# Optimization experiments

Hardware: AMD Instinct MI355X
Metric: run time of the kernel (lower is better)

The kernel has to match this reference:

```python
import jax, jax.numpy as jnp
import numpy as np

N_NODES = 100000
N_EDGES = 3200000
G_EDGES = 1600000
D_FEAT = 256
K_CLUSTERS = 16
COLLAPSE_REG = 0.1


def setup_inputs() -> dict:
    key = jax.random.key(0)
    ks = jax.random.split(key, 12)
    inp = {
        'features': jax.random.normal(ks[0], (N_NODES, D_FEAT), dtype=jnp.float32),
        'W': jax.random.normal(ks[1], (D_FEAT, K_CLUSTERS), dtype=jnp.float32) / np.sqrt(D_FEAT),
        'b': jnp.zeros((K_CLUSTERS,), dtype=jnp.float32),
        'adj_src': jax.random.randint(ks[2], (N_EDGES,), 0, N_NODES, dtype=jnp.int32),
        'adj_dst': jax.random.randint(ks[3], (N_EDGES,), 0, N_NODES, dtype=jnp.int32),
        'adj_val': jax.random.uniform(ks[4], (N_EDGES,), dtype=jnp.float32),
        'g1_src': jax.random.randint(ks[5], (G_EDGES,), 0, N_NODES, dtype=jnp.int32),
        'g1_dst': jax.random.randint(ks[6], (G_EDGES,), 0, N_NODES, dtype=jnp.int32),
        'g1_val': jax.random.uniform(ks[7], (G_EDGES,), dtype=jnp.float32),
        'g2_src': jax.random.randint(ks[8], (G_EDGES,), 0, N_NODES, dtype=jnp.int32),
        'g2_dst': jax.random.randint(ks[9], (G_EDGES,), 0, N_NODES, dtype=jnp.int32),
        'g2_val': jax.random.uniform(ks[10], (G_EDGES,), dtype=jnp.float32),
        'lamda': 1,
    }
    return inp


def _spmm(src, dst, val, X, n):
    # (sparse A) @ X where A[src, dst] = val : out[i] = sum_j A[i,j] X[j]
    return jax.ops.segment_sum(val[:, None] * X[dst], src, num_segments=n)


def _col_degrees(src, dst, val, n):
    # tf.sparse.reduce_sum(A, axis=0): column sums
    return jax.ops.segment_sum(val, dst, num_segments=n)


def reference(features, W, b, adj_src, adj_dst, adj_val,
              g1_src, g1_dst, g1_val, g2_src, g2_dst, g2_val, lamda):
    n = features.shape[0]
    k = W.shape[1]
    # soft cluster assignments  [n, k]
    S = jax.nn.softmax(features @ W + b, axis=1)
    cluster_sizes = jnp.sum(S, axis=0)            # [k]
    S_pool = S / cluster_sizes                    # [n, k]

    # full-graph modularity
    deg = _col_degrees(adj_src, adj_dst, adj_val, n)  # [n]
    m = jnp.sum(deg)                                  # total edge weight
    AS = _spmm(adj_src, adj_dst, adj_val, S, n)       # [n, k]
    graph_pooled = AS.T @ S                           # [k, k]
    dS = deg @ S                                      # [k] = S^T deg
    normalizer = jnp.outer(dS, dS) / 2.0 / m          # [k, k]
    spectral_loss = -jnp.trace(graph_pooled - normalizer) / 2.0 / m

    # per-group modularity Q_g
    def group_Q(src, dst, val):
        gdeg = _col_degrees(src, dst, val, n)
        gm = jnp.sum(gdeg)
        safe_gm = jnp.where(gm > 0, gm, 1.0)
        gAS = _spmm(src, dst, val, S, n)
        g_pooled = gAS.T @ S
        gdS = gdeg @ S
        g_norm = jnp.outer(gdS, gdS) / 2.0 / safe_gm
        Qg = jnp.trace(g_pooled - g_norm) / 2.0 / m
        return jnp.where(gm > 0, Qg, 0.0), gm

    Q1, m1 = group_Q(g1_src, g1_dst, g1_val)
    Q2, m2 = group_Q(g2_src, g2_dst, g2_val)
    Q_min = jnp.minimum(Q1, Q2)
    g_edges_mean = (m1 + m2) / 2.0
    edge_ratio = m / (g_edges_mean + 1e-8)
    fairness_loss = edge_ratio * (-Q_min)

    collapse_loss = (jnp.linalg.norm(cluster_sizes) / n) * jnp.sqrt(jnp.float32(k)) - 1.0

    total_loss = spectral_loss + lamda * fairness_loss + COLLAPSE_REG * collapse_loss

    features_pooled = jax.nn.selu(S_pool.T @ features)  # [k, d]
    return features_pooled, S, total_loss
```

## Files before the change

### kernel.cpp

```cpp
#include <hip/hip_runtime.h>
#include <cstddef>
#include <cstdint>


#define G1_MAX   1024
#define EGRID    2048
#define NSEG     16
#define OFF_E    0
#define SZ_E     (3 * 18 * EGRID)
#define OFF_R    (OFF_E + SZ_E)
#define OFF_G    (OFF_R + 4112)
#define OFF_F8   (OFF_G + 64)

#define TROWS    32
#define RPAD2    134

#define BLK0     384
#define BLK12    192

typedef int      iv4 __attribute__((ext_vector_type(4)));
typedef float    fv4 __attribute__((ext_vector_type(4)));
typedef _Float16 hh;
typedef hh       h2  __attribute__((ext_vector_type(2)));

#if __has_builtin(__builtin_amdgcn_cvt_pk_f32_fp8)
#define HW_FP8 1
#endif

__device__ __forceinline__ h2 bch2(unsigned u) { return __builtin_bit_cast(h2, u); }

__device__ __forceinline__ float fdot2(h2 a, h2 b, float c)
{
#if __has_builtin(__builtin_amdgcn_fdot2)
    return __builtin_amdgcn_fdot2(a, b, c, false);
#else
    return fmaf((float)a[0], (float)b[0], fmaf((float)a[1], (float)b[1], c));
#endif
}

__device__ __forceinline__ h2 pk16(float x, float y)
{
#if __has_builtin(__builtin_amdgcn_cvt_pkrtz)
    return __builtin_bit_cast(h2, __builtin_amdgcn_cvt_pkrtz(x, y));
#else
    h2 r; r[0] = (hh)x; r[1] = (hh)y; return r;
#endif
}

__device__ __forceinline__ unsigned f32_to_e4m3(float f)
{
    unsigned bits = __float_as_uint(f);
    unsigned s = bits >> 31;
    int e32 = (int)((bits >> 23) & 255);
    unsigned m23 = bits & 0x7FFFFF;
    int e = e32 - 120;
    unsigned out;
    if (e32 == 0) out = 0;
    else if (e <= 0) {
        float av = fabsf(f);
        int q = (int)(av * 512.0f + 0.5f);
        out = (unsigned)q;
    } else if (e > 15) out = (15u << 3) | 6u;
    else {
        unsigned m3 = (m23 + 0x80000u) >> 20;
        if (m3 == 8u) { m3 = 0u; ++e; if (e > 15) { e = 15; m3 = 6u; } }
        out = ((unsigned)e << 3) | m3;
    }
    return out | (s << 7);
}

__device__ __forceinline__ void decode16(uint4 r, float* o, const float* lut)
{
#ifdef HW_FP8
    #pragma unroll
    for (int j = 0; j < 4; ++j) {
        unsigned u = (&r.x)[j];
        auto lo = __builtin_amdgcn_cvt_pk_f32_fp8(u, false);
        auto hi = __builtin_amdgcn_cvt_pk_f32_fp8(u, true);
        o[4*j]   = lo[0]; o[4*j+1] = lo[1];
        o[4*j+2] = hi[0]; o[4*j+3] = hi[1];
    }
#else
    #pragma unroll
    for (int j = 0; j < 4; ++j) {
        unsigned u = (&r.x)[j];
        #pragma unroll
        for (int q = 0; q < 4; ++q)
            o[4*j+q] = lut[(u >> (8*q)) & 255];
    }
#endif
}

__global__ void __launch_bounds__(256)
k_rows(const float* __restrict__ F, const float* __restrict__ W,
       const float* __restrict__ b, float* __restrict__ S_out,
       unsigned* __restrict__ S_f8, float* __restrict__ ws_P, int n, int n_tiles)
{
    __shared__ h2    Wt_h2[16][RPAD2];
    __shared__ h2    rows_h2[TROWS][RPAD2];
    __shared__ float S_lds[TROWS][17];
    __shared__ float cs_red[256];

    const int t = threadIdx.x;

    for (int idx = t; idx < 2048; idx += 256) {
        int k = idx & 15, p = idx >> 4;
        Wt_h2[k][p] = pk16(W[(2*p) * 16 + k], W[(2*p + 1) * 16 + k]);
    }

    const float bk = b[t & 15];
    const int rl = t >> 4;
    const int kl = t & 15;
    const int kp = t & 15;
    const int cp = t >> 4;

    h2 Pa[8];
    #pragma unroll
    for (int j = 0; j < 8; ++j) Pa[j] = pk16(0.f, 0.f);
    float cs_acc = 0.f;
    __syncthreads();

    for (int tile = blockIdx.x; tile < n_tiles; tile += gridDim.x) {
        const int row0 = tile * TROWS;
        const float4* F4 = (const float4*)(F + (size_t)row0 * 256);
        #pragma unroll
        for (int q = 0; q < 8; ++q) {
            int idx = t + (q << 8);
            int r = idx >> 6, c4 = idx & 63;
            float4 v = {0.f, 0.f, 0.f, 0.f};
            if (row0 + r < n) v = F4[idx];
            rows_h2[r][c4 * 2]     = pk16(v.x, v.y);
            rows_h2[r][c4 * 2 + 1] = pk16(v.z, v.w);
        }
        __syncthreads();

        float a0 = 0.f, a1 = 0.f;
        #pragma unroll 8
        for (int dd = 0; dd < 32; ++dd) {
            uint4 wv = *(const uint4*)&Wt_h2[kl][dd << 2];
            uint4 r0 = *(const uint4*)&rows_h2[rl][dd << 2];
            uint4 r1 = *(const uint4*)&rows_h2[rl + 16][dd << 2];
            #pragma unroll
            for (int j = 0; j < 4; ++j) {
                h2 wj = bch2((&wv.x)[j]);
                a0 = fdot2(wj, bch2((&r0.x)[j]), a0);
                a1 = fdot2(wj, bch2((&r1.x)[j]), a1);
            }
        }
        a0 += bk; a1 += bk;

        float mx0 = a0, mx1 = a1;
        #pragma unroll
        for (int o = 8; o; o >>= 1) {
            mx0 = fmaxf(mx0, __shfl_xor(mx0, o, 16));
            mx1 = fmaxf(mx1, __shfl_xor(mx1, o, 16));
        }
        float e0 = __expf(a0 - mx0), e1 = __expf(a1 - mx1);
        float s0 = e0, s1 = e1;
        #pragma unroll
        for (int o = 8; o; o >>= 1) {
            s0 += __shfl_xor(s0, o, 16);
            s1 += __shfl_xor(s1, o, 16);
        }
        float sv0 = e0 / s0, sv1 = e1 / s1;

        const bool v0 = (row0 + rl) < n;
        const bool v1 = (row0 + rl + 16) < n;
        if (v0) { S_out[(((size_t)(row0 + rl)) << 4) + kl] = sv0; cs_acc += sv0; }
        if (v1) { S_out[(((size_t)(row0 + rl + 16)) << 4) + kl] = sv1; cs_acc += sv1; }
        S_lds[rl][kl]      = v0 ? sv0 : 0.f;
        S_lds[rl + 16][kl] = v1 ? sv1 : 0.f;
        __syncthreads();

        if (t < 128) {
            int r = t >> 2, c = t & 3;
            int row = row0 + r;
            if (row < n) {
                unsigned u = f32_to_e4m3(S_lds[r][4*c])
                           | (f32_to_e4m3(S_lds[r][4*c+1]) << 8)
                           | (f32_to_e4m3(S_lds[r][4*c+2]) << 16)
                           | (f32_to_e4m3(S_lds[r][4*c+3]) << 24);
                S_f8[((size_t)row << 2) + c] = u;
            }
        }

        #pragma unroll 4
        for (int r = 0; r < TROWS; ++r) {
            float sv = S_lds[r][kp];
            h2 svh = pk16(sv, sv);
            uint4 fa = *(const uint4*)&rows_h2[r][cp << 3];
            uint4 fb = *(const uint4*)&rows_h2[r][(cp << 3) + 4];
            #pragma unroll
            for (int j = 0; j < 4; ++j) {
                Pa[j]     = svh * bch2((&fa.x)[j]) + Pa[j];
                Pa[4 + j] = svh * bch2((&fb.x)[j]) + Pa[4 + j];
            }
        }
        __syncthreads();
    }

    {
        float o16[16];
        #pragma unroll
        for (int j = 0; j < 8; ++j) {
            o16[2*j]     = (float)Pa[j][0];
            o16[2*j + 1] = (float)Pa[j][1];
        }
        float* dst = ws_P + (size_t)blockIdx.x * 4112 + kp * 256 + (cp << 4);
        #pragma unroll
        for (int j = 0; j < 4; ++j)
            *(float4*)&dst[4*j] = make_float4(o16[4*j], o16[4*j+1], o16[4*j+2], o16[4*j+3]);
    }
    cs_red[t] = cs_acc;
    __syncthreads();
    if (t < 16) {
        float ssum = 0.f;
        #pragma unroll
        for (int i = 0; i < 16; ++i) ssum += cs_red[t + (i << 4)];
        ws_P[(size_t)blockIdx.x * 4112 + 4096 + t] = ssum;
    }
}

__global__ void __launch_bounds__(256)
k_reduce(const float* __restrict__ ws_P, float* __restrict__ ws_red, int nb)
{
    const int seg  = blockIdx.x & (NSEG - 1);
    const int jblk = blockIdx.x / NSEG;
    const int idx  = jblk * 256 + threadIdx.x;
    if (idx >= 4112) return;
    const int chunk = (nb + NSEG - 1) / NSEG;
    const int b0 = seg * chunk;
    const int b1 = min(nb, b0 + chunk);
    float s = 0.f;
    for (int bb = b0; bb < b1; ++bb)
        s += ws_P[(size_t)bb * 4112 + idx];
    atomicAdd(&ws_red[idx], s);
}

__global__ void __launch_bounds__(256, 2)
k_edge(const int* __restrict__ src0, const int* __restrict__ dst0,
       const float* __restrict__ val0, int n0,
       const int* __restrict__ src1, const int* __restrict__ dst1,
       const float* __restrict__ val1, int n1,
       const int* __restrict__ src2, const int* __restrict__ dst2,
       const float* __restrict__ val2, int n2,
       const uint4* __restrict__ S8, float* __restrict__ ws_e,
       int b0, int b1)
{
#ifndef HW_FP8
    __shared__ float lut[256];
    if (threadIdx.x < 256) {
        int i = threadIdx.x;
        int e_ = (i >> 3) & 15, m_ = i & 7, s_ = i >> 7;
        float v = e_ ? ldexpf((float)(8 + m_), e_ - 10) : ldexpf((float)m_, -9);
        lut[i] = s_ ? -v : v;
    }
    __syncthreads();
    const float* lutp = lut;
#else
    const float* lutp = nullptr;
#endif

    int g, bb, nblk, nE;
    const int* src; const int* dst; const float* val;
    if ((int)blockIdx.x < b0)      { g = 0; bb = blockIdx.x;      nblk = b0;             src = src0; dst = dst0; val = val0; nE = n0; }
    else if ((int)blockIdx.x < b1) { g = 1; bb = blockIdx.x - b0; nblk = b1 - b0;        src = src1; dst = dst1; val = val1; nE = n1; }
    else                           { g = 2; bb = blockIdx.x - b1; nblk = gridDim.x - b1; src = src2; dst = dst2; val = val2; nE = n2; }

    float m_acc = 0.f, tr_acc = 0.f;
    float gds[16];
    #pragma unroll
    for (int k = 0; k < 16; ++k) gds[k] = 0.f;

    const int nv = nE >> 3;
    const iv4* s4 = (const iv4*)src;
    const iv4* d4 = (const iv4*)dst;
    const fv4* v4 = (const fv4*)val;
    const int stride = nblk * 256;

    for (int i = bb * 256 + threadIdx.x; i < nv; i += stride) {
        iv4 sa = __builtin_nontemporal_load(&s4[2*i]);
        iv4 sb = __builtin_nontemporal_load(&s4[2*i+1]);
        iv4 da = __builtin_nontemporal_load(&d4[2*i]);
        iv4 db = __builtin_nontemporal_load(&d4[2*i+1]);
        fv4 va = __builtin_nontemporal_load(&v4[2*i]);
        fv4 vb = __builtin_nontemporal_load(&v4[2*i+1]);
        int   is[8] = {sa[0], sa[1], sa[2], sa[3], sb[0], sb[1], sb[2], sb[3]};
        int   id[8] = {da[0], da[1], da[2], da[3], db[0], db[1], db[2], db[3]};
        float vv[8] = {va[0], va[1], va[2], va[3], vb[0], vb[1], vb[2], vb[3]};
        uint4 rs[8], rd[8];
        #pragma unroll
        for (int e = 0; e < 8; ++e) {
            rs[e] = S8[is[e]];
            rd[e] = S8[id[e]];
        }
        #pragma unroll
        for (int e = 0; e < 8; ++e) {
            float sv[16], dv[16];
            decode16(rs[e], sv, lutp);
            decode16(rd[e], dv, lutp);
            float v = vv[e];
            float dot = 0.f;
            #pragma unroll
            for (int k = 0; k < 16; ++k) dot = fmaf(sv[k], dv[k], dot);
            m_acc += v;
            tr_acc = fmaf(v, dot, tr_acc);
            #pragma unroll
            for (int k = 0; k < 16; ++k) gds[k] = fmaf(v, dv[k], gds[k]);
        }
    }

    if (bb == 0) {
        int e = (nv << 3) + threadIdx.x;
        if (e < nE) {
            float sv[16], dv[16];
            decode16(S8[src[e]], sv, lutp);
            decode16(S8[dst[e]], dv, lutp);
            float v = val[e];
            float dot = 0.f;
            #pragma unroll
            for (int k = 0; k < 16; ++k) dot = fmaf(sv[k], dv[k], dot);
            m_acc += v;
            tr_acc = fmaf(v, dot, tr_acc);
            #pragma unroll
            for (int k = 0; k < 16; ++k) gds[k] = fmaf(v, dv[k], gds[k]);
        }
    }

    #pragma unroll
    for (int o = 32; o; o >>= 1) {
        m_acc  += __shfl_xor(m_acc, o);
        tr_acc += __shfl_xor(tr_acc, o);
        #pragma unroll
        for (int k = 0; k < 16; ++k) gds[k] += __shfl_xor(gds[k], o);
    }
    __shared__ float wred[4][18];
    const int wid = threadIdx.x >> 6, lane = threadIdx.x & 63;
    if (lane == 0) {
        wred[wid][0] = m_acc; wred[wid][1] = tr_acc;
        #pragma unroll
        for (int k = 0; k < 16; ++k) wred[wid][2 + k] = gds[k];
    }
    __syncthreads();
    if (threadIdx.x < 18) {
        float s = wred[0][threadIdx.x] + wred[1][threadIdx.x]
                + wred[2][threadIdx.x] + wred[3][threadIdx.x];
        ws_e[(size_t)g * 18 * EGRID + (size_t)threadIdx.x * EGRID + bb] = s;
    }
}

__global__ void __launch_bounds__(256)
k_ereduce(const float* __restrict__ ws_e, float* __restrict__ G54,
          int g0, int g1, int g2)
{
    const int p = blockIdx.x;
    const int g = p / 18, slot = p % 18;
    int grids[3] = {g0, g1, g2};
    const int gb = grids[g];
    const float* base = ws_e + (size_t)g * 18 * EGRID + (size_t)slot * EGRID;

    const int t = threadIdx.x;
    float s = 0.f;
    for (int bb = t; bb < gb; bb += 256) s += base[bb];
    #pragma unroll
    for (int o = 32; o; o >>= 1) s += __shfl_xor(s, o);

    __shared__ float wr[4];
    if ((t & 63) == 0) wr[t >> 6] = s;
    __syncthreads();
    if (t == 0) G54[p] = wr[0] + wr[1] + wr[2] + wr[3];
}

__global__ void __launch_bounds__(256)
k_final(const float* __restrict__ ws_red, const float* __restrict__ G54,
        const void* __restrict__ lamda_ptr, float* __restrict__ out, int n)
{
    __shared__ float G[54];
    const int t = threadIdx.x;
    if (t < 54) G[t] = G54[t];
    __syncthreads();

    const float* P  = ws_red;
    const float* cs = ws_red + 4096;

    const float scale = 1.0507009873554805f;
    const float alpha = 1.6732632423543772f;
    for (int idx = t; idx < 4096; idx += 256) {
        int k = idx >> 8;
        float x = P[idx] / cs[k];
        float y = x > 0.f ? scale * x : scale * alpha * (expf(x) - 1.f);
        out[idx] = y;
    }

    if (t == 0) {
        int   li = *(const int*)lamda_ptr;
        float lf = *(const float*)lamda_ptr;
        float lamda = (li > -100000 && li < 100000) ? (float)li : lf;

        float m = G[0], trA = G[1];
        float ds2 = 0.f;
        for (int k = 0; k < 16; ++k) ds2 += G[2 + k] * G[2 + k];
        float spectral = -(trA - ds2 / (2.f * m)) / (2.f * m);

        float Q[2], gm[2];
        for (int g = 0; g < 2; ++g) {
            const float* Gg = G + 18 * (g + 1);
            float mg = Gg[0], trg = Gg[1];
            float gds2 = 0.f;
            for (int k = 0; k < 16; ++k) gds2 += Gg[2 + k] * Gg[2 + k];
            float safe = mg > 0.f ? mg : 1.f;
            float q = (trg - gds2 / (2.f * safe)) / (2.f * m);
            Q[g]  = mg > 0.f ? q : 0.f;
            gm[g] = mg;
        }
        float Qmin = fminf(Q[0], Q[1]);
        float gmean = 0.5f * (gm[0] + gm[1]);
        float fairness = (m / (gmean + 1e-8f)) * (-Qmin);

        float csn = 0.f;
        for (int k = 0; k < 16; ++k) csn += cs[k] * cs[k];
        float collapse = (sqrtf(csn) / (float)n) * 4.f - 1.f;

        out[4096 + (size_t)n * 16] = spectral + lamda * fairness + 0.1f * collapse;
    }
}

extern "C" void kernel_launch(void* const* d_in, const int* in_sizes, int n_in,
                              void* d_out, int out_size, void* d_ws, size_t ws_size,
                              hipStream_t stream)
{
    const float* F       = (const float*)d_in[0];
    const float* W       = (const float*)d_in[1];
    const float* b       = (const float*)d_in[2];
    const int*   adj_src = (const int*)d_in[3];
    const int*   adj_dst = (const int*)d_in[4];
    const float* adj_val = (const float*)d_in[5];
    const int*   g1_src  = (const int*)d_in[6];
    const int*   g1_dst  = (const int*)d_in[7];
    const float* g1_val  = (const float*)d_in[8];
    const int*   g2_src  = (const int*)d_in[9];
    const int*   g2_dst  = (const int*)d_in[10];
    const float* g2_val  = (const float*)d_in[11];
    const void*  lamda_p = d_in[12];

    const int n  = in_sizes[0] / 256;
    const int nE = in_sizes[3];
    const int n1 = in_sizes[6];
    const int n2 = in_sizes[9];

    float* out   = (float*)d_out;
    float* S_out = out + 4096;

    float* ws   = (float*)d_ws;
    float* ws_e = ws + OFF_E;
    float* ws_r = ws + OFF_R;
    float* ws_g = ws + OFF_G;
    unsigned* S8 = (unsigned*)(ws + OFF_F8);
    const size_t off_p = (size_t)OFF_F8 + (size_t)n * 4;
    float* ws_P = ws + off_p;

    const int n_tiles = (n + TROWS - 1) / TROWS;
    long avail = ((long)(ws_size / 4) - (long)off_p) / 4112;
    int grid1 = n_tiles < G1_MAX ? n_tiles : G1_MAX;
    if (avail < grid1) grid1 = (int)avail;
    if (grid1 < 1) grid1 = 1;

    (void)hipMemsetAsync(ws_r, 0, 4112 * sizeof(float), stream);

    k_rows<<<grid1, 256, 0, stream>>>(F, W, b, S_out, S8, ws_P, n, n_tiles);
    k_reduce<<<17 * NSEG, 256, 0, stream>>>(ws_P, ws_r, grid1);

    const int b0 = BLK0, b1g = BLK12, b2g = BLK12;
    k_edge<<<b0 + b1g + b2g, 256, 0, stream>>>(
        adj_src, adj_dst, adj_val, nE,
        g1_src, g1_dst, g1_val, n1,
        g2_src, g2_dst, g2_val, n2,
        (const uint4*)S8, ws_e, b0, b0 + b1g);

    k_ereduce<<<54, 256, 0, stream>>>(ws_e, ws_g, b0, b1g, b2g);
    k_final<<<1, 256, 0, stream>>>(ws_r, ws_g, lamda_p, out, n);
}
```

Before: 162.3 us.

## Prefetch feature tiles into registers and shrink edge batch for occupancy

The softmax/pooling kernel now loads the next feature tile into registers while the current tile is computed, so global load latency overlaps with compute. The edge kernel processes 4 edges per thread instead of 8 and raises the minimum blocks per SM from 2 to 4. It relies on more resident waves to hide gather latency instead of more per-thread parallelism. Grid sizes for the edge kernel groups are also raised. The staging registers and the tighter launch bounds add register pressure and could cause spills.

```diff
diff --git a/kernel.cpp b/kernel.cpp
--- a/kernel.cpp
+++ b/kernel.cpp
@@ -15,8 +15,8 @@
 #define TROWS    32
 #define RPAD2    134
 
-#define BLK0     384
-#define BLK12    192
+#define BLK0     1024
+#define BLK12    512
 
 typedef int      iv4 __attribute__((ext_vector_type(4)));
 typedef float    fv4 __attribute__((ext_vector_type(4)));
@@ -118,21 +118,35 @@
     #pragma unroll
     for (int j = 0; j < 8; ++j) Pa[j] = pk16(0.f, 0.f);
     float cs_acc = 0.f;
+
+    float4 stg[8];
+    auto load_tile = [&](int tl) {
+        const float4* F4 = (const float4*)(F + (size_t)tl * TROWS * 256);
+        #pragma unroll
+        for (int q = 0; q < 8; ++q) {
+            int idx = t + (q << 8);
+            int r = idx >> 6;
+            float4 z = {0.f, 0.f, 0.f, 0.f};
+            stg[q] = (tl * TROWS + r < n) ? F4[idx] : z;
+        }
+    };
+    if (blockIdx.x < (unsigned)n_tiles) load_tile(blockIdx.x);
     __syncthreads();
 
     for (int tile = blockIdx.x; tile < n_tiles; tile += gridDim.x) {
-        const int row0 = tile * TROWS;
-        const float4* F4 = (const float4*)(F + (size_t)row0 * 256);
         #pragma unroll
         for (int q = 0; q < 8; ++q) {
             int idx = t + (q << 8);
             int r = idx >> 6, c4 = idx & 63;
-            float4 v = {0.f, 0.f, 0.f, 0.f};
-            if (row0 + r < n) v = F4[idx];
-            rows_h2[r][c4 * 2]     = pk16(v.x, v.y);
-            rows_h2[r][c4 * 2 + 1] = pk16(v.z, v.w);
+            rows_h2[r][c4 * 2]     = pk16(stg[q].x, stg[q].y);
+            rows_h2[r][c4 * 2 + 1] = pk16(stg[q].z, stg[q].w);
         }
         __syncthreads();
+
+        {
+            int nt2 = tile + gridDim.x;
+            if (nt2 < n_tiles) load_tile(nt2);
+        }
 
         float a0 = 0.f, a1 = 0.f;
         #pragma unroll 8
@@ -164,17 +178,17 @@
         }
         float sv0 = e0 / s0, sv1 = e1 / s1;
 
-        const bool v0 = (row0 + rl) < n;
-        const bool v1 = (row0 + rl + 16) < n;
-        if (v0) { S_out[(((size_t)(row0 + rl)) << 4) + kl] = sv0; cs_acc += sv0; }
-        if (v1) { S_out[(((size_t)(row0 + rl + 16)) << 4) + kl] = sv1; cs_acc += sv1; }
+        const bool v0 = (tile * TROWS + rl) < n;
+        const bool v1 = (tile * TROWS + rl + 16) < n;
+        if (v0) { S_out[(((size_t)(tile * TROWS + rl)) << 4) + kl] = sv0; cs_acc += sv0; }
+        if (v1) { S_out[(((size_t)(tile * TROWS + rl + 16)) << 4) + kl] = sv1; cs_acc += sv1; }
         S_lds[rl][kl]      = v0 ? sv0 : 0.f;
         S_lds[rl + 16][kl] = v1 ? sv1 : 0.f;
         __syncthreads();
 
         if (t < 128) {
             int r = t >> 2, c = t & 3;
-            int row = row0 + r;
+            int row = tile * TROWS + r;
             if (row < n) {
                 unsigned u = f32_to_e4m3(S_lds[r][4*c])
                            | (f32_to_e4m3(S_lds[r][4*c+1]) << 8)
@@ -237,7 +251,7 @@
     atomicAdd(&ws_red[idx], s);
 }
 
-__global__ void __launch_bounds__(256, 2)
+__global__ void __launch_bounds__(256, 4)
 k_edge(const int* __restrict__ src0, const int* __restrict__ dst0,
        const float* __restrict__ val0, int n0,
        const int* __restrict__ src1, const int* __restrict__ dst1,
@@ -272,34 +286,28 @@
     #pragma unroll
     for (int k = 0; k < 16; ++k) gds[k] = 0.f;
 
-    const int nv = nE >> 3;
+    const int nv = nE >> 2;
     const iv4* s4 = (const iv4*)src;
     const iv4* d4 = (const iv4*)dst;
     const fv4* v4 = (const fv4*)val;
     const int stride = nblk * 256;
 
     for (int i = bb * 256 + threadIdx.x; i < nv; i += stride) {
-        iv4 sa = __builtin_nontemporal_load(&s4[2*i]);
-        iv4 sb = __builtin_nontemporal_load(&s4[2*i+1]);
-        iv4 da = __builtin_nontemporal_load(&d4[2*i]);
-        iv4 db = __builtin_nontemporal_load(&d4[2*i+1]);
-        fv4 va = __builtin_nontemporal_load(&v4[2*i]);
-        fv4 vb = __builtin_nontemporal_load(&v4[2*i+1]);
-        int   is[8] = {sa[0], sa[1], sa[2], sa[3], sb[0], sb[1], sb[2], sb[3]};
-        int   id[8] = {da[0], da[1], da[2], da[3], db[0], db[1], db[2], db[3]};
-        float vv[8] = {va[0], va[1], va[2], va[3], vb[0], vb[1], vb[2], vb[3]};
-        uint4 rs[8], rd[8];
-        #pragma unroll
-        for (int e = 0; e < 8; ++e) {
-            rs[e] = S8[is[e]];
-            rd[e] = S8[id[e]];
-        }
-        #pragma unroll
-        for (int e = 0; e < 8; ++e) {
+        iv4 sa = __builtin_nontemporal_load(&s4[i]);
+        iv4 da = __builtin_nontemporal_load(&d4[i]);
+        fv4 va = __builtin_nontemporal_load(&v4[i]);
+        uint4 rs[4], rd[4];
+        #pragma unroll
+        for (int e = 0; e < 4; ++e) {
+            rs[e] = S8[sa[e]];
+            rd[e] = S8[da[e]];
+        }
+        #pragma unroll
+        for (int e = 0; e < 4; ++e) {
             float sv[16], dv[16];
             decode16(rs[e], sv, lutp);
             decode16(rd[e], dv, lutp);
-            float v = vv[e];
+            float v = va[e];
             float dot = 0.f;
             #pragma unroll
             for (int k = 0; k < 16; ++k) dot = fmaf(sv[k], dv[k], dot);
@@ -311,7 +319,7 @@
     }
 
     if (bb == 0) {
-        int e = (nv << 3) + threadIdx.x;
+        int e = (nv << 2) + threadIdx.x;
         if (e < nE) {
             float sv[16], dv[16];
             decode16(S8[src[e]], sv, lutp);
```

Measured after the change: 153.2 us. -5.6%, faster.
